# Performance work log

Measured on AMD Instinct MI355X. Metric: run time of the kernel, lower is better.

## Reference

```python
import jax, jax.numpy as jnp
import numpy as np

EPS = 1e-12  # torch F.normalize eps

def _l2norm(t):
    # normalize over last axis (N), clamp norm like torch.nn.functional.normalize
    n = jnp.linalg.norm(t, axis=-1, keepdims=True)
    return t / jnp.maximum(n, EPS)

def setup_inputs() -> dict:
    key = jax.random.key(0)
    ks = jax.random.split(key, 4)
    B, N, D, H = 8, 4096, 768, 16
    x = jax.random.normal(ks[0], (B, N, D), dtype=jnp.float32)
    w_qkv = jax.random.normal(ks[1], (D, 3 * D), dtype=jnp.float32) * (D ** -0.5)
    temperature = jnp.ones((H, 1, 1), dtype=jnp.float32)
    w_proj = jax.random.normal(ks[2], (D, D), dtype=jnp.float32) * (D ** -0.5)
    b_proj = jnp.zeros((D,), dtype=jnp.float32)
    return {"x": x, "w_qkv": w_qkv, "temperature": temperature,
            "w_proj": w_proj, "b_proj": b_proj}

def reference(x, w_qkv, temperature, w_proj, b_proj):
    B, N, D = x.shape
    H = temperature.shape[0]
    C = D // H
    # qkv linear (no bias), split last dim as (3, H, C), move to (3, B, H, C, N)
    qkv = (x @ w_qkv).reshape(B, N, 3, H, C).transpose(2, 0, 3, 4, 1)
    q, k, v = qkv[0], qkv[1], qkv[2]            # each [B, H, C, N]
    q = _l2norm(q)
    k = _l2norm(k)
    # cross-covariance attention: small CxC matrix per head
    attn = jnp.einsum('bhcn,bhdn->bhcd', q, k) * temperature  # [B,H,C,C]
    attn = jax.nn.softmax(attn, axis=-1)
    out = jnp.einsum('bhcd,bhdn->bhcn', attn, v)  # [B,H,C,N]
    out = out.transpose(0, 3, 1, 2).reshape(B, N, D)  # B N (H C)
    return out @ w_proj + b_proj
```

## Files before the change

### kernel.cpp

```cpp
#include <hip/hip_runtime.h>
#include <stdint.h>

typedef __attribute__((ext_vector_type(4))) float          f32x4;
typedef __attribute__((ext_vector_type(8))) short          bf16x8;
typedef __attribute__((ext_vector_type(8))) unsigned short u16x8;
typedef __attribute__((ext_vector_type(4))) unsigned short u16x4;

static __device__ __forceinline__ unsigned short f2bf(float f){
  uint32_t u = __builtin_bit_cast(uint32_t, f);
  u += 0x7FFFu + ((u >> 16) & 1u);
  return (unsigned short)(u >> 16);
}
static __device__ __forceinline__ float bf2f(unsigned short h){
  uint32_t u = ((uint32_t)h) << 16;
  return __builtin_bit_cast(float, u);
}

__global__ void k_cvt(const float* __restrict__ in, unsigned short* __restrict__ out, long n){
  long i = ((long)blockIdx.x * blockDim.x + threadIdx.x) * 8;
  if (i >= n) return;
  const f32x4* p = (const f32x4*)(in + i);
  f32x4 a = p[0], b = p[1];
  u16x8 o;
  #pragma unroll
  for (int j = 0; j < 4; j++){ o[j] = f2bf(a[j]); o[4+j] = f2bf(b[j]); }
  *(u16x8*)(out + i) = o;
}

__global__ void k_cvtwv(const float* __restrict__ w, unsigned short* __restrict__ out){
  const long idx = ((long)blockIdx.x * blockDim.x + threadIdx.x) * 8;
  const int e = (int)(idx / 768), hd = (int)(idx - (long)e * 768);
  const float* s = w + (long)e * 2304 + 1536 + hd;
  f32x4 a = *(const f32x4*)s, b = *(const f32x4*)(s + 4);
  u16x8 o;
  #pragma unroll
  for (int j = 0; j < 4; j++){ o[j] = f2bf(a[j]); o[4+j] = f2bf(b[j]); }
  *(u16x8*)(out + idx) = o;
}

__global__ void k_tconv(const float* __restrict__ in, unsigned short* __restrict__ out, int R, int C){
  __shared__ float tl[64][65];
  const int c0 = blockIdx.x * 64, r0 = blockIdx.y * 64;
  const int t = threadIdx.x;
  {
    const int lr = t >> 2, lc = (t & 3) * 16;
    const f32x4* s = (const f32x4*)(in + (long)(r0 + lr) * C + c0 + lc);
    #pragma unroll
    for (int q = 0; q < 4; q++){
      f32x4 v = s[q];
      #pragma unroll
      for (int j = 0; j < 4; j++) tl[lr][lc + q*4 + j] = v[j];
    }
  }
  __syncthreads();
  {
    const int oc = t >> 2, orr = (t & 3) * 16;
    u16x8 o0, o1;
    #pragma unroll
    for (int i = 0; i < 8; i++){ o0[i] = f2bf(tl[orr + i][oc]); o1[i] = f2bf(tl[orr + 8 + i][oc]); }
    u16x8* dst = (u16x8*)(out + (long)(c0 + oc) * R + r0 + orr);
    dst[0] = o0; dst[1] = o1;
  }
}

static __device__ __forceinline__ int mapW(int j){
  const int isK = (j >= 768);
  const int jj = j - isK * 768;
  const int h = jj / 48, c = jj - h * 48;
  return (h >> 1) * 192 + (h & 1) * 96 + isK * 48 + c;
}
__global__ void k_tconvQK(const float* __restrict__ in, unsigned short* __restrict__ out){
  __shared__ float tl[64][65];
  const int c0 = blockIdx.x * 64, r0 = blockIdx.y * 64;
  const int t = threadIdx.x;
  {
    const int lr = t >> 2, lc = (t & 3) * 16;
    const f32x4* s = (const f32x4*)(in + (long)(r0 + lr) * 2304 + c0 + lc);
    #pragma unroll
    for (int q = 0; q < 4; q++){
      f32x4 v = s[q];
      #pragma unroll
      for (int j = 0; j < 4; j++) tl[lr][lc + q*4 + j] = v[j];
    }
  }
  __syncthreads();
  {
    const int oc = t >> 2, orr = (t & 3) * 16;
    u16x8 o0, o1;
    #pragma unroll
    for (int i = 0; i < 8; i++){ o0[i] = f2bf(tl[orr + i][oc]); o1[i] = f2bf(tl[orr + 8 + i][oc]); }
    u16x8* dst = (u16x8*)(out + (long)mapW(c0 + oc) * 768 + r0 + orr);
    dst[0] = o0; dst[1] = o1;
  }
}


static __device__ __forceinline__ bf16x8 ldfrag(const char* slot, int row, int ko){
  const int k2 = (ko ^ (row >> 1)) & 3;
  return *(const bf16x8*)(slot + row*64 + k2*16);
}

static __device__ __forceinline__ void stageA512(const unsigned short* __restrict__ G, int row0, int ke,
                                                 char* slot, int t){
  const int r  = t >> 2;
  const int ko = (t & 3) ^ ((r >> 1) & 3);
  const char* src = (const char*)(G + (long)(row0 + r) * 768 + ke + ko * 8);
  char* dst = slot + (t & 0x1C0) * 16;
  __builtin_amdgcn_global_load_lds((const __attribute__((address_space(1))) unsigned int*)src,
                                   (__attribute__((address_space(3))) unsigned int*)dst, 16, 0, 0);
}
static __device__ __forceinline__ void stageB512(const unsigned short* __restrict__ G, int row0, int ke,
                                                 char* slot, int t){
  #pragma unroll
  for (int l = 0; l < 2; l++){
    const int r  = l*128 + (t >> 2);
    const int ko = (t & 3) ^ ((r >> 1) & 3);
    const char* src = (const char*)(G + (long)(row0 + r) * 768 + ke + ko * 8);
    char* dst = slot + l*8192 + (t & 0x1C0) * 16;
    __builtin_amdgcn_global_load_lds((const __attribute__((address_space(1))) unsigned int*)src,
                                     (__attribute__((address_space(3))) unsigned int*)dst, 16, 0, 0);
  }
}

static __device__ __forceinline__ void stageA384(const unsigned short* __restrict__ G, int row0, int ke,
                                                 char* slot, int t){
  {
    const int r  = t >> 2;
    const int ko = (t & 3) ^ ((r >> 1) & 3);
    const char* src = (const char*)(G + (long)(row0 + r) * 768 + ke + ko * 8);
    char* dst = slot + (t & 0x1C0) * 16;
    __builtin_amdgcn_global_load_lds((const __attribute__((address_space(1))) unsigned int*)src,
                                     (__attribute__((address_space(3))) unsigned int*)dst, 16, 0, 0);
  }
  if (t < 128){
    const int r  = 96 + (t >> 2);
    const int ko = (t & 3) ^ ((r >> 1) & 3);
    const char* src = (const char*)(G + (long)(row0 + r) * 768 + ke + ko * 8);
    char* dst = slot + 6144 + (t & 0x1C0) * 16;
    __builtin_amdgcn_global_load_lds((const __attribute__((address_space(1))) unsigned int*)src,
                                     (__attribute__((address_space(3))) unsigned int*)dst, 16, 0, 0);
  }
}
static __device__ __forceinline__ void stageB384(const unsigned short* __restrict__ G, int row0, int ke,
                                                 char* slot, int t){
  #pragma unroll
  for (int l = 0; l < 2; l++){
    const int r  = l*96 + (t >> 2);
    const int ko = (t & 3) ^ ((r >> 1) & 3);
    const char* src = (const char*)(G + (long)(row0 + r) * 768 + ke + ko * 8);
    char* dst = slot + l*6144 + (t & 0x1C0) * 16;
    __builtin_amdgcn_global_load_lds((const __attribute__((address_space(1))) unsigned int*)src,
                                     (__attribute__((address_space(3))) unsigned int*)dst, 16, 0, 0);
  }
}

#define VM0 asm volatile("s_waitcnt vmcnt(0)" ::: "memory")
#define VM3 asm volatile("s_waitcnt vmcnt(3)" ::: "memory")
#define GATEQK { if (w < 2) asm volatile("s_waitcnt vmcnt(4)" ::: "memory");   \
                 else       asm volatile("s_waitcnt vmcnt(3)" ::: "memory"); }

#define PHASE1(CUR, STAGE_STMT, WAIT_STMT) do {                                \
    bf16x8 af[4], bq[4];                                                       \
    _Pragma("unroll")                                                          \
    for (int ni = 0; ni < 4; ni++)                                             \
      bq[ni] = ldfrag(sB[CUR], wn*64 + ni*16 + arow, ko);                      \
    _Pragma("unroll")                                                          \
    for (int mi = 0; mi < 4; mi++)                                             \
      af[mi] = ldfrag(sA[CUR], wm64 + mi*16 + arow, ko);                       \
    __builtin_amdgcn_s_barrier();                                              \
    __builtin_amdgcn_s_setprio(1);                                             \
    _Pragma("unroll")                                                          \
    for (int mi = 0; mi < 4; mi++)                                             \
      _Pragma("unroll")                                                        \
      for (int ni = 0; ni < 4; ni++)                                           \
        acc[mi][ni] = __builtin_amdgcn_mfma_f32_16x16x32_bf16(                 \
            af[mi], bq[ni], acc[mi][ni], 0, 0, 0);                             \
    __builtin_amdgcn_s_setprio(0);                                             \
    STAGE_STMT;                                                                \
    WAIT_STMT;                                                                 \
    __builtin_amdgcn_s_barrier();                                              \
  } while(0)

__global__ __launch_bounds__(384, 3)
void k_gemmQK(const unsigned short* __restrict__ A, const unsigned short* __restrict__ BT,
              float* __restrict__ Spart, float* __restrict__ nrmp)
{
  __shared__ __attribute__((aligned(16))) char lds[61440];
  const int o  = blockIdx.x;
  const int wg = (o & 7) * 256 + (o >> 3);
  const int jt = wg & 7, mt = wg >> 3;
  const int m0 = mt * 128, j0 = jt * 192;
  const int t = threadIdx.x, lane = t & 63, w = t >> 6;
  const int wm = w >> 2 & 1;
  const int wmr = (w < 3) ? 0 : 1;
  const int wn  = (w < 3) ? w : w - 3;
  const int wm64 = wmr * 64;
  const int arow = lane & 15, ko = lane >> 4;
  (void)wm;

  char* const sA[3] = {lds,          lds + 8192,          lds + 16384};
  char* const sB[3] = {lds + 24576,  lds + 24576 + 12288, lds + 24576 + 24576};

  f32x4 acc[4][4] = {};

  stageA384(A, m0, 0,  sA[0], t);  stageB384(BT, j0, 0,  sB[0], t);
  stageA384(A, m0, 32, sA[1], t);  stageB384(BT, j0, 32, sB[1], t);
  GATEQK;
  __builtin_amdgcn_s_barrier();

  #pragma unroll 1
  for (int g = 0; g < 7; ++g){
    const int kb = g * 96;
    PHASE1(0, { stageA384(A, m0, kb+64,  sA[2], t); stageB384(BT, j0, kb+64,  sB[2], t); }, GATEQK);
    PHASE1(1, { stageA384(A, m0, kb+96,  sA[0], t); stageB384(BT, j0, kb+96,  sB[0], t); }, GATEQK);
    PHASE1(2, { stageA384(A, m0, kb+128, sA[1], t); stageB384(BT, j0, kb+128, sB[1], t); }, GATEQK);
  }
  PHASE1(0, { stageA384(A, m0, 736, sA[2], t); stageB384(BT, j0, 736, sB[2], t); }, GATEQK);
  PHASE1(1, { ; }, VM0);
  PHASE1(2, { ; }, ;);

  const int b = m0 >> 12;
  const int chunk = ((m0 & 4095) >> 6) + wmr;
  #pragma unroll
  for (int ni = 0; ni < 4; ni++){
    float ss = 0.f;
    #pragma unroll
    for (int mi = 0; mi < 4; mi++)
      #pragma unroll
      for (int r = 0; r < 4; r++) ss += acc[mi][ni][r] * acc[mi][ni][r];
    ss += __shfl_xor(ss, 16);
    ss += __shfl_xor(ss, 32);
    if (lane < 16){
      const int jr = wn*64 + ni*16 + lane;
      const int hl = jr / 96, rem = jr - hl*96;
      const int isK = (rem >= 48), c = rem - isK*48;
      const int prow = isK*6144 + (b*16 + jt*2 + hl)*48 + c;
      nrmp[(long)prow*64 + chunk] = ss;
    }
  }
  __syncthreads();
  #pragma unroll
  for (int mi = 0; mi < 4; mi++){
    #pragma unroll
    for (int ni = 0; ni < 4; ni++){
      const int j = wn*64 + ni*16 + (lane & 15);
      const int n = wm64 + mi*16 + (lane >> 4)*4;
      u16x4 pk;
      #pragma unroll
      for (int r = 0; r < 4; r++) pk[r] = f2bf(acc[mi][ni][r]);
      *(u16x4*)(lds + (long)j*272 + n*2) = pk;
    }
  }
  __syncthreads();
  {
    const int hl = (w < 3) ? 0 : 1;
    const int ci = (w < 3) ? w : w - 3;
    f32x4 accs[3] = {};
    #pragma unroll
    for (int kt = 0; kt < 128; kt += 32){
      const bf16x8 aq = *(const bf16x8*)(lds + (long)(hl*96 + ci*16 + (lane & 15))*272
                                             + (kt + (lane >> 4)*8)*2);
      #pragma unroll
      for (int di = 0; di < 3; di++){
        const bf16x8 bk = *(const bf16x8*)(lds + (long)(hl*96 + 48 + di*16 + (lane & 15))*272
                                               + (kt + (lane >> 4)*8)*2);
        accs[di] = __builtin_amdgcn_mfma_f32_16x16x32_bf16(aq, bk, accs[di], 0, 0, 0);
      }
    }
    const int ksp = (m0 & 4095) >> 7;
    float* Sb = Spart + ((long)ksp*128 + b*16 + jt*2 + hl) * 2304;
    #pragma unroll
    for (int di = 0; di < 3; di++)
      #pragma unroll
      for (int r = 0; r < 4; r++){
        const int c = ci*16 + (lane >> 4)*4 + r;
        const int d = di*16 + (lane & 15);
        Sb[c*48 + d] = accs[di][r];
      }
  }
}

__global__ __launch_bounds__(512, 4)
void k_gemmP(const unsigned short* __restrict__ A, const unsigned short* __restrict__ BT,
             float* __restrict__ OUTF, const float* __restrict__ bias)
{
  __shared__ __attribute__((aligned(16))) char lds[73728];
  const int o  = blockIdx.x;
  const int wg = (o & 7) * 96 + (o >> 3);
  const int jt = wg % 3, mt = wg / 3;
  const int m0 = mt * 128, j0 = jt * 256;
  const int t = threadIdx.x, lane = t & 63, w = t >> 6;
  const int wm = w >> 2, wn = w & 3;
  const int wm64 = wm * 64;
  const int arow = lane & 15, ko = lane >> 4;
  const unsigned short* BTb = BT + ((long)(m0 >> 12)) * 589824;

  char* const sA[3] = {lds,          lds + 8192,          lds + 16384};
  char* const sB[3] = {lds + 24576,  lds + 24576 + 16384, lds + 24576 + 32768};

  f32x4 acc[4][4] = {};

  stageA512(A, m0, 0,  sA[0], t);  stageB512(BTb, j0, 0,  sB[0], t);
  stageA512(A, m0, 32, sA[1], t);  stageB512(BTb, j0, 32, sB[1], t);
  VM3;
  __builtin_amdgcn_s_barrier();

  #pragma unroll 1
  for (int g = 0; g < 7; ++g){
    const int kb = g * 96;
    PHASE1(0, { stageA512(A, m0, kb+64,  sA[2], t); stageB512(BTb, j0, kb+64,  sB[2], t); }, VM3);
    PHASE1(1, { stageA512(A, m0, kb+96,  sA[0], t); stageB512(BTb, j0, kb+96,  sB[0], t); }, VM3);
    PHASE1(2, { stageA512(A, m0, kb+128, sA[1], t); stageB512(BTb, j0, kb+128, sB[1], t); }, VM3);
  }
  PHASE1(0, { stageA512(A, m0, 736, sA[2], t); stageB512(BTb, j0, 736, sB[2], t); }, VM3);
  PHASE1(1, { ; }, VM0);
  PHASE1(2, { ; }, ;);

  #pragma unroll
  for (int mi = 0; mi < 4; mi++){
    #pragma unroll
    for (int ni = 0; ni < 4; ni++){
      const int jc = j0 + wn*64 + ni*16 + (lane & 15);
      const float bv = bias[jc];
      const long mr = (long)m0 + wm64 + mi*16 + (lane >> 4)*4;
      #pragma unroll
      for (int r = 0; r < 4; r++) OUTF[(mr + r) * 768 + jc] = acc[mi][ni][r] + bv;
    }
  }
}

__global__ void k_softmax(const float* __restrict__ Spart, const float* __restrict__ nrmp,
                          const float* __restrict__ temp, unsigned short* __restrict__ attnT)
{
  __shared__ float Ss[2304];
  __shared__ float invq[48], invk[48];
  const int bh = blockIdx.x, h = bh & 15;
  const int t = threadIdx.x;
  f32x4 a0[9];
  #pragma unroll
  for (int v = 0; v < 9; v++) a0[v] = f32x4{0.f,0.f,0.f,0.f};
  for (int p = 0; p < 32; p++){
    const f32x4* src = (const f32x4*)(Spart + ((long)p*128 + bh)*2304);
    #pragma unroll
    for (int v = 0; v < 9; v++) a0[v] += src[v*64 + t];
  }
  #pragma unroll
  for (int v = 0; v < 9; v++) *(f32x4*)(Ss + (v*64 + t)*4) = a0[v];
  if (t < 48){
    float sq = 0.f, sk = 0.f;
    const float* pq = nrmp + (long)(bh*48 + t) * 64;
    const float* pk = nrmp + (long)(6144 + bh*48 + t) * 64;
    #pragma unroll
    for (int i = 0; i < 64; i++){ sq += pq[i]; sk += pk[i]; }
    invq[t] = 1.0f / fmaxf(sqrtf(sq), 1e-12f);
    invk[t] = 1.0f / fmaxf(sqrtf(sk), 1e-12f);
  }
  __syncthreads();
  if (t < 48){
    const int c = t;
    const float scq = invq[c] * temp[h];
    float row[48];
    #pragma unroll
    for (int d = 0; d < 48; d++) row[d] = Ss[c*48 + d] * scq * invk[d];
    float mx = -1e30f;
    #pragma unroll
    for (int d = 0; d < 48; d++) mx = fmaxf(mx, row[d]);
    float s = 0.f;
    #pragma unroll
    for (int d = 0; d < 48; d++){ row[d] = expf(row[d] - mx); s += row[d]; }
    const float inv = 1.0f / s;
    unsigned short* ob = attnT + (long)bh * 48 * 64;
    #pragma unroll
    for (int d = 0; d < 48; d++) ob[d*64 + c] = f2bf(row[d] * inv);
    u16x8 z = {};
    *(u16x8*)(ob + c*64 + 48) = z;
    *(u16x8*)(ob + c*64 + 56) = z;
  }
}

__global__ __launch_bounds__(256)
void k_wmod2(const unsigned short* __restrict__ WpT, const unsigned short* __restrict__ attnT,
             unsigned short* __restrict__ WmodT)
{
  const int j0 = blockIdx.x * 256, h = blockIdx.y, b = blockIdx.z;
  const int t = threadIdx.x, lane = t & 63, w = t >> 6;
  const unsigned short* wp = WpT + h * 48;
  const unsigned short* ab = attnT + ((long)(b*16 + h)) * 48 * 64;
  f32x4 acc[4][3] = {};
  #pragma unroll
  for (int kt = 0; kt < 64; kt += 32){
    bf16x8 bfr[3];
    #pragma unroll
    for (int ni = 0; ni < 3; ni++)
      bfr[ni] = *(const bf16x8*)(ab + (ni*16 + (lane & 15))*64 + kt + (lane >> 4)*8);
    #pragma unroll
    for (int mi = 0; mi < 4; mi++){
      const int j = j0 + w*64 + mi*16 + (lane & 15);
      bf16x8 a = *(const bf16x8*)(wp + (long)j*768 + kt + (lane >> 4)*8);
      #pragma unroll
      for (int ni = 0; ni < 3; ni++)
        acc[mi][ni] = __builtin_amdgcn_mfma_f32_16x16x32_bf16(a, bfr[ni], acc[mi][ni], 0, 0, 0);
    }
  }
  #pragma unroll
  for (int mi = 0; mi < 4; mi++)
    #pragma unroll
    for (int ni = 0; ni < 3; ni++)
      #pragma unroll
      for (int r = 0; r < 4; r++){
        const int j = j0 + w*64 + mi*16 + (lane >> 4)*4 + r;
        const int d = ni*16 + (lane & 15);
        WmodT[(long)b*589824 + (long)j*768 + h*48 + d] = f2bf(acc[mi][ni][r]);
      }
}

__global__ __launch_bounds__(256)
void k_comb(const unsigned short* __restrict__ A, const unsigned short* __restrict__ BT,
            unsigned short* __restrict__ OUT)
{
  __shared__ unsigned short As[128 * 32];
  __shared__ unsigned short Bs[128 * 32];
  const int m0 = blockIdx.y * 128;
  const int j0 = blockIdx.x * 128;
  const int t = threadIdx.x;
  const int lane = t & 63;
  const int w = t >> 6, wm = w >> 1, wn = w & 1;

  f32x4 acc[4][4] = {};

  for (int kt = 0; kt < 768; kt += 32){
    if (kt) __syncthreads();
    #pragma unroll
    for (int i = 0; i < 2; i++){
      const char* ga = (const char*)A  + (long)(m0 + i*64 + (t >> 2)) * 1536 + kt*2 + (t & 3) * 16;
      const char* gb = (const char*)BT + (long)(j0 + i*64 + (t >> 2)) * 1536 + kt*2 + (t & 3) * 16;
      char* la = (char*)As + i*4096 + (t & 0xC0) * 16;
      char* lb = (char*)Bs + i*4096 + (t & 0xC0) * 16;
      __builtin_amdgcn_global_load_lds((const __attribute__((address_space(1))) unsigned int*)ga,
                                       (__attribute__((address_space(3))) unsigned int*)la, 16, 0, 0);
      __builtin_amdgcn_global_load_lds((const __attribute__((address_space(1))) unsigned int*)gb,
                                       (__attribute__((address_space(3))) unsigned int*)lb, 16, 0, 0);
    }
    __syncthreads();
    bf16x8 af[4], bfr[4];
    #pragma unroll
    for (int mi = 0; mi < 4; mi++)
      af[mi]  = *(const bf16x8*)&As[(wm*64 + mi*16 + (lane & 15)) * 32 + (lane >> 4) * 8];
    #pragma unroll
    for (int ni = 0; ni < 4; ni++)
      bfr[ni] = *(const bf16x8*)&Bs[(wn*64 + ni*16 + (lane & 15)) * 32 + (lane >> 4) * 8];
    #pragma unroll
    for (int mi = 0; mi < 4; mi++)
      #pragma unroll
      for (int ni = 0; ni < 4; ni++)
        acc[mi][ni] = __builtin_amdgcn_mfma_f32_16x16x32_bf16(af[mi], bfr[ni], acc[mi][ni], 0, 0, 0);
  }

  #pragma unroll
  for (int mi = 0; mi < 4; mi++)
    #pragma unroll
    for (int ni = 0; ni < 4; ni++){
      const int jc = j0 + wn*64 + ni*16 + (lane & 15);
      const long mr = (long)m0 + wm*64 + mi*16 + (lane >> 4) * 4;
      #pragma unroll
      for (int r = 0; r < 4; r++) OUT[(mr + r) * 768 + jc] = f2bf(acc[mi][ni][r]);
    }
}

extern "C" void kernel_launch(void* const* d_in, const int* in_sizes, int n_in,
                              void* d_out, int out_size, void* d_ws, size_t ws_size,
                              hipStream_t stream)
{
  (void)in_sizes; (void)n_in; (void)out_size; (void)ws_size;
  const float* x      = (const float*)d_in[0];
  const float* w_qkv  = (const float*)d_in[1];
  const float* temp   = (const float*)d_in[2];
  const float* w_proj = (const float*)d_in[3];
  const float* b_proj = (const float*)d_in[4];
  float* outF = (float*)d_out;

  char* ws = (char*)d_ws;
  size_t off = 0;
  auto alloc = [&](size_t bytes)->char*{ char* p = ws + off; off += (bytes + 255) & ~(size_t)255; return p; };

  unsigned short* x_bf  = (unsigned short*)alloc(50331648);
  unsigned short* WTr   = (unsigned short*)alloc(2359296);
  unsigned short* WpT   = (unsigned short*)alloc(1179648);
  unsigned short* WvB   = (unsigned short*)alloc(1179648);
  float* nrmp           = (float*)alloc(12288L * 64 * 4);
  float* Spart          = (float*)alloc(32L * 128 * 2304 * 4);
  unsigned short* attnT = (unsigned short*)alloc(128L * 48 * 64 * 2);
  unsigned short* WmodT = (unsigned short*)alloc(9437184);
  unsigned short* WcombT= (unsigned short*)alloc(9437184);

  k_cvt<<<12288, 256, 0, stream>>>(x, x_bf, 25165824L);
  k_tconvQK<<<dim3(24, 12), 256, 0, stream>>>(w_qkv, WTr);
  k_tconv<<<dim3(12, 12), 256, 0, stream>>>(w_proj, WpT, 768, 768);
  k_cvtwv<<<288, 256, 0, stream>>>(w_qkv, WvB);
  k_gemmQK<<<2048, 384, 0, stream>>>(x_bf, WTr, Spart, nrmp);
  k_softmax<<<128, 64, 0, stream>>>(Spart, nrmp, temp, attnT);
  k_wmod2<<<dim3(3, 16, 8), 256, 0, stream>>>(WpT, attnT, WmodT);
  k_comb<<<dim3(6, 48), 256, 0, stream>>>(WmodT, WvB, WcombT);
  k_gemmP<<<768, 512, 0, stream>>>(x_bf, WcombT, outF, b_proj);
}
```

Baseline: 245.5 us.

## Compute QK scores via the x Gram matrix instead of full Q/K projection

Replaces the fused QK-projection GEMM, which produced partial CxC scores and norms, with an algebraic route. It first forms the per-batch Gram matrix G = x^T x (768x768) from a transposed bf16 copy of x, then T = G·W_qk. Each q·k score, and the q and k norms, become dot products of T rows with W rows in a small per-head softmax kernel. This drops the large N-dimension reduction over 1536 projected columns and the partial-sum buffers. In exchange it writes an extra transposed copy of x and adds two batched GEMM launches and a bf16-rounded intermediate that may cost accuracy.

New measurement: 285.5 us. +16.3%, slower.

```diff
diff --git a/kernel.cpp b/kernel.cpp
--- a/kernel.cpp
+++ b/kernel.cpp
@@ -16,26 +16,38 @@
   return __builtin_bit_cast(float, u);
 }
 
-__global__ void k_cvt(const float* __restrict__ in, unsigned short* __restrict__ out, long n){
-  long i = ((long)blockIdx.x * blockDim.x + threadIdx.x) * 8;
-  if (i >= n) return;
-  const f32x4* p = (const f32x4*)(in + i);
-  f32x4 a = p[0], b = p[1];
-  u16x8 o;
-  #pragma unroll
-  for (int j = 0; j < 4; j++){ o[j] = f2bf(a[j]); o[4+j] = f2bf(b[j]); }
-  *(u16x8*)(out + i) = o;
-}
-
-__global__ void k_cvtwv(const float* __restrict__ w, unsigned short* __restrict__ out){
-  const long idx = ((long)blockIdx.x * blockDim.x + threadIdx.x) * 8;
-  const int e = (int)(idx / 768), hd = (int)(idx - (long)e * 768);
-  const float* s = w + (long)e * 2304 + 1536 + hd;
-  f32x4 a = *(const f32x4*)s, b = *(const f32x4*)(s + 4);
-  u16x8 o;
-  #pragma unroll
-  for (int j = 0; j < 4; j++){ o[j] = f2bf(a[j]); o[4+j] = f2bf(b[j]); }
-  *(u16x8*)(out + idx) = o;
+__global__ void k_cvtT(const float* __restrict__ in, unsigned short* __restrict__ xbf,
+                       unsigned short* __restrict__ xT){
+  __shared__ float tl[64][65];
+  const int c0 = blockIdx.x * 64, r0 = blockIdx.y * 64;
+  const int t = threadIdx.x;
+  {
+    const int lr = t >> 2, lc = (t & 3) * 16;
+    const f32x4* s = (const f32x4*)(in + (long)(r0 + lr) * 768 + c0 + lc);
+    f32x4 v[4];
+    #pragma unroll
+    for (int q = 0; q < 4; q++){
+      v[q] = s[q];
+      #pragma unroll
+      for (int j = 0; j < 4; j++) tl[lr][lc + q*4 + j] = v[q][j];
+    }
+    u16x8 o0, o1;
+    #pragma unroll
+    for (int j = 0; j < 4; j++){ o0[j] = f2bf(v[0][j]); o0[4+j] = f2bf(v[1][j]);
+                                 o1[j] = f2bf(v[2][j]); o1[4+j] = f2bf(v[3][j]); }
+    u16x8* d = (u16x8*)(xbf + (long)(r0 + lr) * 768 + c0 + lc);
+    d[0] = o0; d[1] = o1;
+  }
+  __syncthreads();
+  {
+    const int oc = t >> 2, orr = (t & 3) * 16;
+    const int b = r0 >> 12, n0 = r0 & 4095;
+    u16x8 o0, o1;
+    #pragma unroll
+    for (int i = 0; i < 8; i++){ o0[i] = f2bf(tl[orr + i][oc]); o1[i] = f2bf(tl[orr + 8 + i][oc]); }
+    u16x8* dst = (u16x8*)(xT + (long)b*3145728 + (long)(c0 + oc)*4096 + n0 + orr);
+    dst[0] = o0; dst[1] = o1;
+  }
 }
 
 __global__ void k_tconv(const float* __restrict__ in, unsigned short* __restrict__ out, int R, int C){
@@ -94,70 +106,60 @@
   }
 }
 
+__global__ void k_cvtwv(const float* __restrict__ w, unsigned short* __restrict__ out){
+  const long idx = ((long)blockIdx.x * blockDim.x + threadIdx.x) * 8;
+  const int e = (int)(idx / 768), hd = (int)(idx - (long)e * 768);
+  const float* s = w + (long)e * 2304 + 1536 + hd;
+  f32x4 a = *(const f32x4*)s, b = *(const f32x4*)(s + 4);
+  u16x8 o;
+  #pragma unroll
+  for (int j = 0; j < 4; j++){ o[j] = f2bf(a[j]); o[4+j] = f2bf(b[j]); }
+  *(u16x8*)(out + idx) = o;
+}
 
 static __device__ __forceinline__ bf16x8 ldfrag(const char* slot, int row, int ko){
   const int k2 = (ko ^ (row >> 1)) & 3;
   return *(const bf16x8*)(slot + row*64 + k2*16);
 }
 
+#define GLL(SRC, DST) __builtin_amdgcn_global_load_lds(                         \
+    (const __attribute__((address_space(1))) unsigned int*)(SRC),               \
+    (__attribute__((address_space(3))) unsigned int*)(DST), 16, 0, 0)
+
 static __device__ __forceinline__ void stageA512(const unsigned short* __restrict__ G, int row0, int ke,
                                                  char* slot, int t){
   const int r  = t >> 2;
-  const int ko = (t & 3) ^ ((r >> 1) & 3);
-  const char* src = (const char*)(G + (long)(row0 + r) * 768 + ke + ko * 8);
-  char* dst = slot + (t & 0x1C0) * 16;
-  __builtin_amdgcn_global_load_lds((const __attribute__((address_space(1))) unsigned int*)src,
-                                   (__attribute__((address_space(3))) unsigned int*)dst, 16, 0, 0);
+  const int k2 = (t & 3) ^ ((r >> 1) & 3);
+  GLL((const char*)(G + (long)(row0 + r) * 768 + ke + k2 * 8), slot + (t & 0x1C0) * 16);
 }
 static __device__ __forceinline__ void stageB512(const unsigned short* __restrict__ G, int row0, int ke,
                                                  char* slot, int t){
   #pragma unroll
   for (int l = 0; l < 2; l++){
     const int r  = l*128 + (t >> 2);
-    const int ko = (t & 3) ^ ((r >> 1) & 3);
-    const char* src = (const char*)(G + (long)(row0 + r) * 768 + ke + ko * 8);
-    char* dst = slot + l*8192 + (t & 0x1C0) * 16;
-    __builtin_amdgcn_global_load_lds((const __attribute__((address_space(1))) unsigned int*)src,
-                                     (__attribute__((address_space(3))) unsigned int*)dst, 16, 0, 0);
-  }
-}
-
-static __device__ __forceinline__ void stageA384(const unsigned short* __restrict__ G, int row0, int ke,
-                                                 char* slot, int t){
-  {
-    const int r  = t >> 2;
-    const int ko = (t & 3) ^ ((r >> 1) & 3);
-    const char* src = (const char*)(G + (long)(row0 + r) * 768 + ke + ko * 8);
-    char* dst = slot + (t & 0x1C0) * 16;
-    __builtin_amdgcn_global_load_lds((const __attribute__((address_space(1))) unsigned int*)src,
-                                     (__attribute__((address_space(3))) unsigned int*)dst, 16, 0, 0);
-  }
-  if (t < 128){
-    const int r  = 96 + (t >> 2);
-    const int ko = (t & 3) ^ ((r >> 1) & 3);
-    const char* src = (const char*)(G + (long)(row0 + r) * 768 + ke + ko * 8);
-    char* dst = slot + 6144 + (t & 0x1C0) * 16;
-    __builtin_amdgcn_global_load_lds((const __attribute__((address_space(1))) unsigned int*)src,
-                                     (__attribute__((address_space(3))) unsigned int*)dst, 16, 0, 0);
-  }
-}
-static __device__ __forceinline__ void stageB384(const unsigned short* __restrict__ G, int row0, int ke,
-                                                 char* slot, int t){
+    const int k2 = (t & 3) ^ ((r >> 1) & 3);
+    GLL((const char*)(G + (long)(row0 + r) * 768 + ke + k2 * 8), slot + l*8192 + (t & 0x1C0) * 16);
+  }
+}
+
+static __device__ __forceinline__ void stA64(const unsigned short* __restrict__ G, int row0, int ke,
+                                             int pitch, char* slot, int t){
+  const int r  = t >> 2;
+  const int k2 = (t & 3) ^ ((r >> 1) & 3);
+  GLL((const char*)(G + (long)(row0 + r) * pitch + ke + k2 * 8), slot + (t & 0xC0) * 16);
+}
+static __device__ __forceinline__ void stB128(const unsigned short* __restrict__ G, int row0, int ke,
+                                              int pitch, char* slot, int t){
   #pragma unroll
   for (int l = 0; l < 2; l++){
-    const int r  = l*96 + (t >> 2);
-    const int ko = (t & 3) ^ ((r >> 1) & 3);
-    const char* src = (const char*)(G + (long)(row0 + r) * 768 + ke + ko * 8);
-    char* dst = slot + l*6144 + (t & 0x1C0) * 16;
-    __builtin_amdgcn_global_load_lds((const __attribute__((address_space(1))) unsigned int*)src,
-                                     (__attribute__((address_space(3))) unsigned int*)dst, 16, 0, 0);
+    const int r  = l*64 + (t >> 2);
+    const int k2 = (t & 3) ^ ((r >> 1) & 3);
+    GLL((const char*)(G + (long)(row0 + r) * pitch + ke + k2 * 8), slot + l*4096 + (t & 0xC0) * 16);
   }
 }
 
 #define VM0 asm volatile("s_waitcnt vmcnt(0)" ::: "memory")
 #define VM3 asm volatile("s_waitcnt vmcnt(3)" ::: "memory")
-#define GATEQK { if (w < 2) asm volatile("s_waitcnt vmcnt(4)" ::: "memory");   \
-                 else       asm volatile("s_waitcnt vmcnt(3)" ::: "memory"); }
 
 #define PHASE1(CUR, STAGE_STMT, WAIT_STMT) do {                                \
     bf16x8 af[4], bq[4];                                                       \
@@ -181,102 +183,89 @@
     __builtin_amdgcn_s_barrier();                                              \
   } while(0)
 
-__global__ __launch_bounds__(384, 3)
-void k_gemmQK(const unsigned short* __restrict__ A, const unsigned short* __restrict__ BT,
-              float* __restrict__ Spart, float* __restrict__ nrmp)
+#define PH_BT(CUR, STAGE_STMT, WAIT_STMT) do {                                 \
+    bf16x8 af[2], bq[4];                                                       \
+    _Pragma("unroll")                                                          \
+    for (int ni = 0; ni < 4; ni++)                                             \
+      bq[ni] = ldfrag(sB[CUR], wn*64 + ni*16 + arow, ko);                      \
+    _Pragma("unroll")                                                          \
+    for (int mi = 0; mi < 2; mi++)                                             \
+      af[mi] = ldfrag(sA[CUR], wm*32 + mi*16 + arow, ko);                      \
+    __builtin_amdgcn_s_barrier();                                              \
+    __builtin_amdgcn_s_setprio(1);                                             \
+    _Pragma("unroll")                                                          \
+    for (int mi = 0; mi < 2; mi++)                                             \
+      _Pragma("unroll")                                                        \
+      for (int ni = 0; ni < 4; ni++)                                           \
+        acc[mi][ni] = __builtin_amdgcn_mfma_f32_16x16x32_bf16(                 \
+            af[mi], bq[ni], acc[mi][ni], 0, 0, 0);                             \
+    __builtin_amdgcn_s_setprio(0);                                             \
+    STAGE_STMT;                                                                \
+    WAIT_STMT;                                                                 \
+    __builtin_amdgcn_s_barrier();                                              \
+  } while(0)
+
+template<int NKT>
+__global__ __launch_bounds__(256, 4)
+void k_bt(const unsigned short* __restrict__ A, long Abstride, int Apitch,
+          const unsigned short* __restrict__ B, long Bbstride, int Bpitch,
+          unsigned short* __restrict__ OUT, long Obstride, int NJT)
 {
-  __shared__ __attribute__((aligned(16))) char lds[61440];
-  const int o  = blockIdx.x;
-  const int wg = (o & 7) * 256 + (o >> 3);
-  const int jt = wg & 7, mt = wg >> 3;
-  const int m0 = mt * 128, j0 = jt * 192;
+  __shared__ __attribute__((aligned(16))) char lds[36864];
+  const int o = blockIdx.x;
+  const int b = o & 7;
+  const int rem = o >> 3;
+  const int mt = rem / NJT, jt = rem - mt * NJT;
+  const int m0 = mt * 64, j0 = jt * 128;
   const int t = threadIdx.x, lane = t & 63, w = t >> 6;
-  const int wm = w >> 2 & 1;
-  const int wmr = (w < 3) ? 0 : 1;
-  const int wn  = (w < 3) ? w : w - 3;
-  const int wm64 = wmr * 64;
+  const int wm = w >> 1, wn = w & 1;
   const int arow = lane & 15, ko = lane >> 4;
-  (void)wm;
-
-  char* const sA[3] = {lds,          lds + 8192,          lds + 16384};
-  char* const sB[3] = {lds + 24576,  lds + 24576 + 12288, lds + 24576 + 24576};
-
-  f32x4 acc[4][4] = {};
-
-  stageA384(A, m0, 0,  sA[0], t);  stageB384(BT, j0, 0,  sB[0], t);
-  stageA384(A, m0, 32, sA[1], t);  stageB384(BT, j0, 32, sB[1], t);
-  GATEQK;
+  const unsigned short* Ab = A + (long)b * Abstride;
+  const unsigned short* Bb = B + (long)b * Bbstride;
+  unsigned short* Ob = OUT + (long)b * Obstride;
+
+  char* const sA[3] = {lds,          lds + 4096,          lds + 8192};
+  char* const sB[3] = {lds + 12288,  lds + 12288 + 8192,  lds + 12288 + 16384};
+
+  f32x4 acc[2][4] = {};
+
+  stA64(Ab, m0, 0,  Apitch, sA[0], t);  stB128(Bb, j0, 0,  Bpitch, sB[0], t);
+  stA64(Ab, m0, 32, Apitch, sA[1], t);  stB128(Bb, j0, 32, Bpitch, sB[1], t);
+  VM3;
   __builtin_amdgcn_s_barrier();
 
+  constexpr int F = (NKT - 2) / 3;
   #pragma unroll 1
-  for (int g = 0; g < 7; ++g){
+  for (int g = 0; g < F; ++g){
     const int kb = g * 96;
-    PHASE1(0, { stageA384(A, m0, kb+64,  sA[2], t); stageB384(BT, j0, kb+64,  sB[2], t); }, GATEQK);
-    PHASE1(1, { stageA384(A, m0, kb+96,  sA[0], t); stageB384(BT, j0, kb+96,  sB[0], t); }, GATEQK);
-    PHASE1(2, { stageA384(A, m0, kb+128, sA[1], t); stageB384(BT, j0, kb+128, sB[1], t); }, GATEQK);
-  }
-  PHASE1(0, { stageA384(A, m0, 736, sA[2], t); stageB384(BT, j0, 736, sB[2], t); }, GATEQK);
-  PHASE1(1, { ; }, VM0);
-  PHASE1(2, { ; }, ;);
-
-  const int b = m0 >> 12;
-  const int chunk = ((m0 & 4095) >> 6) + wmr;
-  #pragma unroll
-  for (int ni = 0; ni < 4; ni++){
-    float ss = 0.f;
-    #pragma unroll
-    for (int mi = 0; mi < 4; mi++)
-      #pragma unroll
-      for (int r = 0; r < 4; r++) ss += acc[mi][ni][r] * acc[mi][ni][r];
-    ss += __shfl_xor(ss, 16);
-    ss += __shfl_xor(ss, 32);
-    if (lane < 16){
-      const int jr = wn*64 + ni*16 + lane;
-      const int hl = jr / 96, rem = jr - hl*96;
-      const int isK = (rem >= 48), c = rem - isK*48;
-      const int prow = isK*6144 + (b*16 + jt*2 + hl)*48 + c;
-      nrmp[(long)prow*64 + chunk] = ss;
-    }
-  }
-  __syncthreads();
-  #pragma unroll
-  for (int mi = 0; mi < 4; mi++){
+    PH_BT(0, { stA64(Ab, m0, kb+64,  Apitch, sA[2], t); stB128(Bb, j0, kb+64,  Bpitch, sB[2], t); }, VM3);
+    PH_BT(1, { stA64(Ab, m0, kb+96,  Apitch, sA[0], t); stB128(Bb, j0, kb+96,  Bpitch, sB[0], t); }, VM3);
+    PH_BT(2, { stA64(Ab, m0, kb+128, Apitch, sA[1], t); stB128(Bb, j0, kb+128, Bpitch, sB[1], t); }, VM3);
+  }
+  #pragma unroll
+  for (int p = 3*F; p < NKT; ++p){
+    const int cur = p % 3;
+    if (p + 2 < NKT){
+      const int ke = (p + 2) * 32, sl = (p + 2) % 3;
+      PH_BT(cur, { stA64(Ab, m0, ke, Apitch, sA[sl], t); stB128(Bb, j0, ke, Bpitch, sB[sl], t); }, VM3);
+    } else if (p == NKT - 2){
+      PH_BT(cur, { ; }, VM0);
+    } else {
+      PH_BT(cur, { ; }, ;);
+    }
+  }
+
+  #pragma unroll
+  for (int mi = 0; mi < 2; mi++){
     #pragma unroll
     for (int ni = 0; ni < 4; ni++){
-      const int j = wn*64 + ni*16 + (lane & 15);
-      const int n = wm64 + mi*16 + (lane >> 4)*4;
+      const int jc = j0 + wn*64 + ni*16 + (lane & 15);
+      const int mr = m0 + wm*32 + mi*16 + (lane >> 4)*4;
       u16x4 pk;
       #pragma unroll
       for (int r = 0; r < 4; r++) pk[r] = f2bf(acc[mi][ni][r]);
-      *(u16x4*)(lds + (long)j*272 + n*2) = pk;
-    }
-  }
-  __syncthreads();
-  {
-    const int hl = (w < 3) ? 0 : 1;
-    const int ci = (w < 3) ? w : w - 3;
-    f32x4 accs[3] = {};
-    #pragma unroll
-    for (int kt = 0; kt < 128; kt += 32){
-      const bf16x8 aq = *(const bf16x8*)(lds + (long)(hl*96 + ci*16 + (lane & 15))*272
-                                             + (kt + (lane >> 4)*8)*2);
-      #pragma unroll
-      for (int di = 0; di < 3; di++){
-        const bf16x8 bk = *(const bf16x8*)(lds + (long)(hl*96 + 48 + di*16 + (lane & 15))*272
-                                               + (kt + (lane >> 4)*8)*2);
-        accs[di] = __builtin_amdgcn_mfma_f32_16x16x32_bf16(aq, bk, accs[di], 0, 0, 0);
-      }
-    }
-    const int ksp = (m0 & 4095) >> 7;
-    float* Sb = Spart + ((long)ksp*128 + b*16 + jt*2 + hl) * 2304;
-    #pragma unroll
-    for (int di = 0; di < 3; di++)
-      #pragma unroll
-      for (int r = 0; r < 4; r++){
-        const int c = ci*16 + (lane >> 4)*4 + r;
-        const int d = di*16 + (lane & 15);
-        Sb[c*48 + d] = accs[di][r];
-      }
+      *(u16x4*)(Ob + (long)jc*768 + mr) = pk;
+    }
   }
 }
 
@@ -329,39 +318,65 @@
   }
 }
 
-__global__ void k_softmax(const float* __restrict__ Spart, const float* __restrict__ nrmp,
-                          const float* __restrict__ temp, unsigned short* __restrict__ attnT)
+__global__ void k_smax(const unsigned short* __restrict__ Tt, const unsigned short* __restrict__ WTr,
+                       const float* __restrict__ temp, unsigned short* __restrict__ attnT)
 {
-  __shared__ float Ss[2304];
-  __shared__ float invq[48], invk[48];
-  const int bh = blockIdx.x, h = bh & 15;
-  const int t = threadIdx.x;
-  f32x4 a0[9];
-  #pragma unroll
-  for (int v = 0; v < 9; v++) a0[v] = f32x4{0.f,0.f,0.f,0.f};
-  for (int p = 0; p < 32; p++){
-    const f32x4* src = (const f32x4*)(Spart + ((long)p*128 + bh)*2304);
-    #pragma unroll
-    for (int v = 0; v < 9; v++) a0[v] += src[v*64 + t];
-  }
-  #pragma unroll
-  for (int v = 0; v < 9; v++) *(f32x4*)(Ss + (v*64 + t)*4) = a0[v];
-  if (t < 48){
-    float sq = 0.f, sk = 0.f;
-    const float* pq = nrmp + (long)(bh*48 + t) * 64;
-    const float* pk = nrmp + (long)(6144 + bh*48 + t) * 64;
-    #pragma unroll
-    for (int i = 0; i < 64; i++){ sq += pq[i]; sk += pk[i]; }
-    invq[t] = 1.0f / fmaxf(sqrtf(sq), 1e-12f);
-    invk[t] = 1.0f / fmaxf(sqrtf(sk), 1e-12f);
+  __shared__ float Sl[48][52];
+  __shared__ float invk_s[48];
+  const int bh = blockIdx.x, b = bh >> 4, h = bh & 15;
+  const int rowq = (h >> 1) * 192 + (h & 1) * 96, rowk = rowq + 48;
+  const unsigned short* Tb = Tt + (long)b * 1179648;
+  const int lane = threadIdx.x;
+  const int arow = lane & 15, ko = lane >> 4;
+
+  f32x4 acc[3][3] = {};
+  for (int kt = 0; kt < 768; kt += 32){
+    bf16x8 af[3], bfr[3];
+    #pragma unroll
+    for (int ci = 0; ci < 3; ci++)
+      af[ci]  = *(const bf16x8*)(Tb + (long)(rowq + ci*16 + arow)*768 + kt + ko*8);
+    #pragma unroll
+    for (int di = 0; di < 3; di++)
+      bfr[di] = *(const bf16x8*)(WTr + (long)(rowk + di*16 + arow)*768 + kt + ko*8);
+    #pragma unroll
+    for (int ci = 0; ci < 3; ci++)
+      #pragma unroll
+      for (int di = 0; di < 3; di++)
+        acc[ci][di] = __builtin_amdgcn_mfma_f32_16x16x32_bf16(af[ci], bfr[di], acc[ci][di], 0, 0, 0);
+  }
+  #pragma unroll
+  for (int ci = 0; ci < 3; ci++)
+    #pragma unroll
+    for (int di = 0; di < 3; di++)
+      #pragma unroll
+      for (int r = 0; r < 4; r++)
+        Sl[ci*16 + ko*4 + r][di*16 + arow] = acc[ci][di][r];
+
+  float dq = 0.f;
+  if (lane < 48){
+    const unsigned short* tq = Tb  + (long)(rowq + lane)*768;
+    const unsigned short* wq = WTr + (long)(rowq + lane)*768;
+    const unsigned short* tk = Tb  + (long)(rowk + lane)*768;
+    const unsigned short* wk = WTr + (long)(rowk + lane)*768;
+    float dk = 0.f;
+    for (int e = 0; e < 768; e += 8){
+      bf16x8 a = *(const bf16x8*)(tq + e), bq_ = *(const bf16x8*)(wq + e);
+      bf16x8 c = *(const bf16x8*)(tk + e), bk_ = *(const bf16x8*)(wk + e);
+      #pragma unroll
+      for (int j = 0; j < 8; j++){
+        dq += bf2f(((u16x8)a)[j]) * bf2f(((u16x8)bq_)[j]);
+        dk += bf2f(((u16x8)c)[j]) * bf2f(((u16x8)bk_)[j]);
+      }
+    }
+    invk_s[lane] = 1.0f / fmaxf(sqrtf(dk), 1e-12f);
   }
   __syncthreads();
-  if (t < 48){
-    const int c = t;
-    const float scq = invq[c] * temp[h];
+  if (lane < 48){
+    const int c = lane;
+    const float scq = temp[h] / fmaxf(sqrtf(dq), 1e-12f);
     float row[48];
     #pragma unroll
-    for (int d = 0; d < 48; d++) row[d] = Ss[c*48 + d] * scq * invk[d];
+    for (int d = 0; d < 48; d++) row[d] = Sl[c][d] * scq * invk_s[d];
     float mx = -1e30f;
     #pragma unroll
     for (int d = 0; d < 48; d++) mx = fmaxf(mx, row[d]);
@@ -436,10 +451,8 @@
       const char* gb = (const char*)BT + (long)(j0 + i*64 + (t >> 2)) * 1536 + kt*2 + (t & 3) * 16;
       char* la = (char*)As + i*4096 + (t & 0xC0) * 16;
       char* lb = (char*)Bs + i*4096 + (t & 0xC0) * 16;
-      __builtin_amdgcn_global_load_lds((const __attribute__((address_space(1))) unsigned int*)ga,
-                                       (__attribute__((address_space(3))) unsigned int*)la, 16, 0, 0);
-      __builtin_amdgcn_global_load_lds((const __attribute__((address_space(1))) unsigned int*)gb,
-                                       (__attribute__((address_space(3))) unsigned int*)lb, 16, 0, 0);
+      GLL(ga, la);
+      GLL(gb, lb);
     }
     __syncthreads();
     bf16x8 af[4], bfr[4];
@@ -484,21 +497,23 @@
   auto alloc = [&](size_t bytes)->char*{ char* p = ws + off; off += (bytes + 255) & ~(size_t)255; return p; };
 
   unsigned short* x_bf  = (unsigned short*)alloc(50331648);
+  unsigned short* xT    = (unsigned short*)alloc(50331648);
   unsigned short* WTr   = (unsigned short*)alloc(2359296);
   unsigned short* WpT   = (unsigned short*)alloc(1179648);
   unsigned short* WvB   = (unsigned short*)alloc(1179648);
-  float* nrmp           = (float*)alloc(12288L * 64 * 4);
-  float* Spart          = (float*)alloc(32L * 128 * 2304 * 4);
-  unsigned short* attnT = (unsigned short*)alloc(128L * 48 * 64 * 2);
+  unsigned short* G     = (unsigned short*)alloc(9437184);
+  unsigned short* Tt    = (unsigned short*)alloc(18874368);
+  unsigned short* attnT = (unsigned short*)alloc(786432);
   unsigned short* WmodT = (unsigned short*)alloc(9437184);
   unsigned short* WcombT= (unsigned short*)alloc(9437184);
 
-  k_cvt<<<12288, 256, 0, stream>>>(x, x_bf, 25165824L);
+  k_cvtT<<<dim3(12, 512), 256, 0, stream>>>(x, x_bf, xT);
   k_tconvQK<<<dim3(24, 12), 256, 0, stream>>>(w_qkv, WTr);
   k_tconv<<<dim3(12, 12), 256, 0, stream>>>(w_proj, WpT, 768, 768);
   k_cvtwv<<<288, 256, 0, stream>>>(w_qkv, WvB);
-  k_gemmQK<<<2048, 384, 0, stream>>>(x_bf, WTr, Spart, nrmp);
-  k_softmax<<<128, 64, 0, stream>>>(Spart, nrmp, temp, attnT);
+  k_bt<128><<<576, 256, 0, stream>>>(xT, 3145728L, 4096, xT, 3145728L, 4096, G, 589824L, 6);
+  k_bt<24><<<1152, 256, 0, stream>>>(G, 589824L, 768, WTr, 0L, 768, Tt, 1179648L, 12);
+  k_smax<<<128, 64, 0, stream>>>(Tt, WTr, temp, attnT);
   k_wmod2<<<dim3(3, 16, 8), 256, 0, stream>>>(WpT, attnT, WmodT);
   k_comb<<<dim3(6, 48), 256, 0, stream>>>(WmodT, WvB, WcombT);
   k_gemmP<<<768, 512, 0, stream>>>(x_bf, WcombT, outF, b_proj);
```
